# Kernel tuning notes

Hardware: AMD Instinct MI355X
Metric: run time of the kernel (lower is better)

## Reference

```python
import jax, jax.numpy as jnp
import numpy as np

B, T, DE, DR, H = 8192, 8, 512, 1024, 1024


def setup_inputs() -> dict:
    key = jax.random.key(0)
    ks = jax.random.split(key, 8)
    std = 1.0 / np.sqrt(H)
    u = lambda k, shape: jax.random.uniform(k, shape, jnp.float32, -std, std)
    return {
        "entity": jax.random.normal(ks[0], (B, T, DE), jnp.float32),
        "relation": jax.random.normal(ks[1], (B, T, DR), jnp.float32),
        "We": u(ks[2], (H, DE)),
        "be": u(ks[3], (H,)),
        "Wr": u(ks[4], (H, DR)),
        "br": u(ks[5], (H,)),
        "Wh": u(ks[6], (H, H)),
        "bh": u(ks[7], (H,)),
    }


def reference(entity, relation, We, be, Wr, br, Wh, bh):
    # entity: [B, T, DE], relation: [B, T, DR]
    # Precompute time-parallel input projections (linear, math-equivalent to per-step).
    g = (jnp.einsum("btd,hd->bth", entity, We) + be
         + jnp.einsum("btd,hd->bth", relation, Wr) + br)  # [B, T, H]

    def step(h, gt):
        h = jax.nn.relu(gt + h @ Wh.T + bh)  # RNNCell_rel: relu(e2h(e)+r2h(r)+h2h(h))
        return h, h

    h0 = jnp.zeros((entity.shape[0], Wh.shape[0]), entity.dtype)
    hn, outs = jax.lax.scan(step, h0, jnp.transpose(g, (1, 0, 2)))  # outs: [T, B, H]
    output = jnp.transpose(outs, (1, 0, 2))  # [B, T, H] (batch-first)
    need = hn.T  # faithful to hidden[0].transpose(0,1): [H, B]
    return output, need
```

## Files before the change

kernel.cpp:

```cpp
#include <hip/hip_runtime.h>
#include <hip/hip_bf16.h>

#define BB 8192
#define TT 8
#define DEe 512
#define DRr 1024
#define HH 1024
#define KG 1536
#define MG 65536

typedef __attribute__((ext_vector_type(8))) __bf16 bf16x8;
typedef __attribute__((ext_vector_type(4))) __bf16 bf16x4;
typedef __attribute__((ext_vector_type(4))) float f32x4;

__device__ __forceinline__ void gld_lds16(const __bf16* g, __bf16* l) {
    __builtin_amdgcn_global_load_lds(
        (const __attribute__((address_space(1))) void*)g,
        (__attribute__((address_space(3))) void*)l, 16, 0, 0);
}

__global__ void pack_ga(const float* __restrict__ ent, const float* __restrict__ rel,
                        __bf16* __restrict__ ga) {
    const int total = MG * (KG / 4);
    const int stride = gridDim.x * blockDim.x;
    for (int g = blockIdx.x * blockDim.x + threadIdx.x; g < total; g += stride) {
        int m = g / 384;
        int c4 = g - m * 384;
        float4 v;
        if (c4 < 128) v = ((const float4*)ent)[(size_t)m * 128 + c4];
        else          v = ((const float4*)rel)[(size_t)m * 256 + (c4 - 128)];
        bf16x4 o = {(__bf16)v.x, (__bf16)v.y, (__bf16)v.z, (__bf16)v.w};
        *(bf16x4*)(ga + (size_t)m * KG + c4 * 4) = o;
    }
}

__global__ void pack_bw(const float* __restrict__ We, const float* __restrict__ Wr,
                        const float* __restrict__ Wh,
                        __bf16* __restrict__ BW, __bf16* __restrict__ WhP) {
    const int n = blockIdx.y;
    const int sec = blockIdx.x;
    const int i = threadIdx.x;
    float4 v; __bf16* dst;
    if (sec == 0) {
        v = *(const float4*)(We + (size_t)n * DEe + i * 4);
        dst = BW + (size_t)n * KG + i * 4;
    } else if (sec <= 2) {
        int d = (sec - 1) * 512 + i * 4;
        v = *(const float4*)(Wr + (size_t)n * DRr + d);
        dst = BW + (size_t)n * KG + DEe + d;
    } else {
        int d = (sec - 3) * 512 + i * 4;
        v = *(const float4*)(Wh + (size_t)n * HH + d);
        dst = WhP + (size_t)n * HH + d;
    }
    bf16x4 o = {(__bf16)v.x, (__bf16)v.y, (__bf16)v.z, (__bf16)v.w};
    *(bf16x4*)dst = o;
}

__global__ __launch_bounds__(256) void gemm_g(
    const __bf16* __restrict__ A, const __bf16* __restrict__ Bw,
    const float* __restrict__ be, const float* __restrict__ br,
    const float* __restrict__ bh,
    float* __restrict__ out, __bf16* __restrict__ h0) {
    __shared__ __bf16 sA[128 * 32];
    __shared__ __bf16 sB[128 * 32];
    __shared__ float sBias[128];

    const int tid  = threadIdx.x;
    const int lane = tid & 63;
    const int w    = tid >> 6;
    const int bid  = blockIdx.y * 8 + blockIdx.x;
    const int swz  = (bid & 7) * 512 + (bid >> 3);
    const int tileN = (swz & 7) * 128;
    const int tileM = (swz >> 3) * 128;

    if (tid < 128) {
        int n = tileN + tid;
        sBias[tid] = be[n] + br[n] + bh[n];
    }

    const int r0 = (w * 2 + 0) * 16 + (lane >> 2);
    const int r1 = (w * 2 + 1) * 16 + (lane >> 2);
    const int cc = (lane & 3) * 8;
    const __bf16* gA0 = A + (size_t)(tileM + r0) * KG + cc;
    const __bf16* gA1 = A + (size_t)(tileM + r1) * KG + cc;
    const __bf16* gB0 = Bw + (size_t)(tileN + r0) * KG + cc;
    const __bf16* gB1 = Bw + (size_t)(tileN + r1) * KG + cc;
    __bf16* lA0 = sA + (w * 2 + 0) * 512;
    __bf16* lA1 = sA + (w * 2 + 1) * 512;
    __bf16* lB0 = sB + (w * 2 + 0) * 512;
    __bf16* lB1 = sB + (w * 2 + 1) * 512;

    const int wm = (w >> 1) * 64, wn = (w & 1) * 64;
    const int fm = lane & 15, fq = lane >> 4;

    f32x4 acc[4][4];
#pragma unroll
    for (int i = 0; i < 4; i++)
#pragma unroll
        for (int j = 0; j < 4; j++) acc[i][j] = {0.f, 0.f, 0.f, 0.f};

    for (int k0 = 0; k0 < KG; k0 += 32) {
        gld_lds16(gA0 + k0, lA0);
        gld_lds16(gA1 + k0, lA1);
        gld_lds16(gB0 + k0, lB0);
        gld_lds16(gB1 + k0, lB1);
        __syncthreads();
        bf16x8 af[4], bf[4];
#pragma unroll
        for (int mf = 0; mf < 4; mf++)
            af[mf] = *(const bf16x8*)&sA[(wm + mf * 16 + fm) * 32 + fq * 8];
#pragma unroll
        for (int nf = 0; nf < 4; nf++)
            bf[nf] = *(const bf16x8*)&sB[(wn + nf * 16 + fm) * 32 + fq * 8];
#pragma unroll
        for (int mf = 0; mf < 4; mf++)
#pragma unroll
            for (int nf = 0; nf < 4; nf++)
                acc[mf][nf] = __builtin_amdgcn_mfma_f32_16x16x32_bf16(
                    af[mf], bf[nf], acc[mf][nf], 0, 0, 0);
        __syncthreads();
    }

#pragma unroll
    for (int mf = 0; mf < 4; mf++) {
#pragma unroll
        for (int nf = 0; nf < 4; nf++) {
            f32x4 v = acc[mf][nf];
            const int nl = wn + nf * 16 + fm;
            const int n  = tileN + nl;
            const int m0 = tileM + wm + mf * 16 + fq * 4;
            const float bias = sBias[nl];
            const bool t0row = ((m0 & 7) == 0);
#pragma unroll
            for (int r = 0; r < 4; r++) {
                float x = v[r] + bias;
                size_t m = (size_t)(m0 + r);
                if (t0row && r == 0) {
                    float hv = x > 0.f ? x : 0.f;
                    out[m * HH + n] = hv;
                    h0[(m >> 3) * HH + n] = (__bf16)hv;
                } else {
                    out[m * HH + n] = x;
                }
            }
        }
    }
}

__global__ __launch_bounds__(256) void gemm_step(
    const __bf16* __restrict__ A, const __bf16* __restrict__ Bw,
    float* __restrict__ out, __bf16* __restrict__ hn,
    float* __restrict__ need, int t) {
    __shared__ __bf16 sA[128 * 32];
    __shared__ __bf16 sB[128 * 32];

    const int tid  = threadIdx.x;
    const int lane = tid & 63;
    const int w    = tid >> 6;
    const int bid  = blockIdx.y * 8 + blockIdx.x;
    const int swz  = (bid & 7) * 64 + (bid >> 3);
    const int tileN = (swz & 7) * 128;
    const int tileM = (swz >> 3) * 128;

    const int r0 = (w * 2 + 0) * 16 + (lane >> 2);
    const int r1 = (w * 2 + 1) * 16 + (lane >> 2);
    const int cc = (lane & 3) * 8;
    const __bf16* gA0 = A + (size_t)(tileM + r0) * HH + cc;
    const __bf16* gA1 = A + (size_t)(tileM + r1) * HH + cc;
    const __bf16* gB0 = Bw + (size_t)(tileN + r0) * HH + cc;
    const __bf16* gB1 = Bw + (size_t)(tileN + r1) * HH + cc;
    __bf16* lA0 = sA + (w * 2 + 0) * 512;
    __bf16* lA1 = sA + (w * 2 + 1) * 512;
    __bf16* lB0 = sB + (w * 2 + 0) * 512;
    __bf16* lB1 = sB + (w * 2 + 1) * 512;

    const int wm = (w >> 1) * 64, wn = (w & 1) * 64;
    const int fm = lane & 15, fq = lane >> 4;

    f32x4 acc[4][4];
#pragma unroll
    for (int i = 0; i < 4; i++)
#pragma unroll
        for (int j = 0; j < 4; j++) acc[i][j] = {0.f, 0.f, 0.f, 0.f};

    for (int k0 = 0; k0 < HH; k0 += 32) {
        gld_lds16(gA0 + k0, lA0);
        gld_lds16(gA1 + k0, lA1);
        gld_lds16(gB0 + k0, lB0);
        gld_lds16(gB1 + k0, lB1);
        __syncthreads();
        bf16x8 af[4], bf[4];
#pragma unroll
        for (int mf = 0; mf < 4; mf++)
            af[mf] = *(const bf16x8*)&sA[(wm + mf * 16 + fm) * 32 + fq * 8];
#pragma unroll
        for (int nf = 0; nf < 4; nf++)
            bf[nf] = *(const bf16x8*)&sB[(wn + nf * 16 + fm) * 32 + fq * 8];
#pragma unroll
        for (int mf = 0; mf < 4; mf++)
#pragma unroll
            for (int nf = 0; nf < 4; nf++)
                acc[mf][nf] = __builtin_amdgcn_mfma_f32_16x16x32_bf16(
                    af[mf], bf[nf], acc[mf][nf], 0, 0, 0);
        __syncthreads();
    }

#pragma unroll
    for (int mf = 0; mf < 4; mf++) {
#pragma unroll
        for (int nf = 0; nf < 4; nf++) {
            f32x4 v = acc[mf][nf];
            const int nl = wn + nf * 16 + fm;
            const int n  = tileN + nl;
            const int m0 = tileM + wm + mf * 16 + fq * 4;
            float hv[4];
#pragma unroll
            for (int r = 0; r < 4; r++) {
                size_t addr = ((size_t)(m0 + r) * TT + t) * HH + n;
                float x = v[r] + out[addr];
                hv[r] = x > 0.f ? x : 0.f;
                out[addr] = hv[r];
                if (hn) hn[(size_t)(m0 + r) * HH + n] = (__bf16)hv[r];
            }
            if (need) {
                f32x4 nv = {hv[0], hv[1], hv[2], hv[3]};
                *(f32x4*)&need[(size_t)n * BB + m0] = nv;
            }
        }
    }
}

extern "C" void kernel_launch(void* const* d_in, const int* in_sizes, int n_in,
                              void* d_out, int out_size, void* d_ws, size_t ws_size,
                              hipStream_t stream) {
    const float* ent = (const float*)d_in[0];
    const float* rel = (const float*)d_in[1];
    const float* We  = (const float*)d_in[2];
    const float* be  = (const float*)d_in[3];
    const float* Wr  = (const float*)d_in[4];
    const float* br  = (const float*)d_in[5];
    const float* Wh  = (const float*)d_in[6];
    const float* bh  = (const float*)d_in[7];

    float* out  = (float*)d_out;
    float* need = out + (size_t)BB * TT * HH;

    char* ws = (char*)d_ws;
    __bf16* GA  = (__bf16*)ws;
    __bf16* BW  = (__bf16*)(ws + (size_t)MG * KG * 2);
    __bf16* WhP = (__bf16*)(ws + (size_t)MG * KG * 2 + (size_t)HH * KG * 2);
    __bf16* hA  = (__bf16*)((char*)WhP + (size_t)HH * HH * 2);
    __bf16* hB  = (__bf16*)((char*)hA + (size_t)BB * HH * 2);
    __bf16* hbuf[2] = {hA, hB};

    pack_bw<<<dim3(5, 1024), 128, 0, stream>>>(We, Wr, Wh, BW, WhP);
    pack_ga<<<dim3(2048), 256, 0, stream>>>(ent, rel, GA);
    gemm_g<<<dim3(8, 512), 256, 0, stream>>>(GA, BW, be, br, bh, out, hA);
    for (int t = 1; t < TT; t++) {
        gemm_step<<<dim3(8, 64), 256, 0, stream>>>(
            hbuf[(t - 1) & 1], WhP, out,
            (t < 7) ? hbuf[t & 1] : nullptr,
            (t == 7) ? need : nullptr, t);
    }
}
```

Baseline: 1.286 ms.

## Fuse recurrent steps into one persistent kernel keeping hidden state in LDS

Replaces the seven per-timestep GEMM launches with a single kernel in which each block owns 32 batch rows, keeps their hidden state in swizzled LDS as bf16, and loops over all timesteps. Wh is pre-packed into a k-major tiled layout so each k-chunk can be streamed into LDS with plain vector loads. This removes the global round-trips of the hidden state and the per-step launch overhead. In exchange, every block re-streams the full Wh on every step (256 blocks, 512 threads, 128KB LDS, one block per CU), which leans heavily on L2 and gives lower MFMA reuse per Wh byte.

```diff
diff --git a/kernel.cpp b/kernel.cpp
--- a/kernel.cpp
+++ b/kernel.cpp
@@ -36,7 +36,7 @@
 
 __global__ void pack_bw(const float* __restrict__ We, const float* __restrict__ Wr,
                         const float* __restrict__ Wh,
-                        __bf16* __restrict__ BW, __bf16* __restrict__ WhP) {
+                        __bf16* __restrict__ BW, __bf16* __restrict__ WhT) {
     const int n = blockIdx.y;
     const int sec = blockIdx.x;
     const int i = threadIdx.x;
@@ -51,7 +51,7 @@
     } else {
         int d = (sec - 3) * 512 + i * 4;
         v = *(const float4*)(Wh + (size_t)n * HH + d);
-        dst = WhP + (size_t)n * HH + d;
+        dst = WhT + (d >> 5) * 32768 + ((d >> 3) & 3) * 8192 + n * 8 + (d & 7);
     }
     bf16x4 o = {(__bf16)v.x, (__bf16)v.y, (__bf16)v.z, (__bf16)v.w};
     *(bf16x4*)dst = o;
@@ -60,8 +60,7 @@
 __global__ __launch_bounds__(256) void gemm_g(
     const __bf16* __restrict__ A, const __bf16* __restrict__ Bw,
     const float* __restrict__ be, const float* __restrict__ br,
-    const float* __restrict__ bh,
-    float* __restrict__ out, __bf16* __restrict__ h0) {
+    const float* __restrict__ bh, float* __restrict__ out) {
     __shared__ __bf16 sA[128 * 32];
     __shared__ __bf16 sB[128 * 32];
     __shared__ float sBias[128];
@@ -106,19 +105,19 @@
         gld_lds16(gB0 + k0, lB0);
         gld_lds16(gB1 + k0, lB1);
         __syncthreads();
-        bf16x8 af[4], bf[4];
+        bf16x8 af[4], bfv[4];
 #pragma unroll
         for (int mf = 0; mf < 4; mf++)
             af[mf] = *(const bf16x8*)&sA[(wm + mf * 16 + fm) * 32 + fq * 8];
 #pragma unroll
         for (int nf = 0; nf < 4; nf++)
-            bf[nf] = *(const bf16x8*)&sB[(wn + nf * 16 + fm) * 32 + fq * 8];
+            bfv[nf] = *(const bf16x8*)&sB[(wn + nf * 16 + fm) * 32 + fq * 8];
 #pragma unroll
         for (int mf = 0; mf < 4; mf++)
 #pragma unroll
             for (int nf = 0; nf < 4; nf++)
                 acc[mf][nf] = __builtin_amdgcn_mfma_f32_16x16x32_bf16(
-                    af[mf], bf[nf], acc[mf][nf], 0, 0, 0);
+                    af[mf], bfv[nf], acc[mf][nf], 0, 0, 0);
         __syncthreads();
     }
 
@@ -137,9 +136,7 @@
                 float x = v[r] + bias;
                 size_t m = (size_t)(m0 + r);
                 if (t0row && r == 0) {
-                    float hv = x > 0.f ? x : 0.f;
-                    out[m * HH + n] = hv;
-                    h0[(m >> 3) * HH + n] = (__bf16)hv;
+                    out[m * HH + n] = x > 0.f ? x : 0.f;
                 } else {
                     out[m * HH + n] = x;
                 }
@@ -148,86 +145,99 @@
     }
 }
 
-__global__ __launch_bounds__(256) void gemm_step(
-    const __bf16* __restrict__ A, const __bf16* __restrict__ Bw,
-    float* __restrict__ out, __bf16* __restrict__ hn,
-    float* __restrict__ need, int t) {
-    __shared__ __bf16 sA[128 * 32];
-    __shared__ __bf16 sB[128 * 32];
+__global__ __launch_bounds__(512, 1) void rnn_local(
+    const __bf16* __restrict__ Bw,
+    float* __restrict__ out, float* __restrict__ need) {
+    __shared__ __bf16 sH[32 * 1024];
+    __shared__ __bf16 sB[32 * 1024];
 
     const int tid  = threadIdx.x;
     const int lane = tid & 63;
     const int w    = tid >> 6;
-    const int bid  = blockIdx.y * 8 + blockIdx.x;
-    const int swz  = (bid & 7) * 64 + (bid >> 3);
-    const int tileN = (swz & 7) * 128;
-    const int tileM = (swz >> 3) * 128;
-
-    const int r0 = (w * 2 + 0) * 16 + (lane >> 2);
-    const int r1 = (w * 2 + 1) * 16 + (lane >> 2);
-    const int cc = (lane & 3) * 8;
-    const __bf16* gA0 = A + (size_t)(tileM + r0) * HH + cc;
-    const __bf16* gA1 = A + (size_t)(tileM + r1) * HH + cc;
-    const __bf16* gB0 = Bw + (size_t)(tileN + r0) * HH + cc;
-    const __bf16* gB1 = Bw + (size_t)(tileN + r1) * HH + cc;
-    __bf16* lA0 = sA + (w * 2 + 0) * 512;
-    __bf16* lA1 = sA + (w * 2 + 1) * 512;
-    __bf16* lB0 = sB + (w * 2 + 0) * 512;
-    __bf16* lB1 = sB + (w * 2 + 1) * 512;
-
-    const int wm = (w >> 1) * 64, wn = (w & 1) * 64;
-    const int fm = lane & 15, fq = lane >> 4;
-
-    f32x4 acc[4][4];
-#pragma unroll
-    for (int i = 0; i < 4; i++)
-#pragma unroll
-        for (int j = 0; j < 4; j++) acc[i][j] = {0.f, 0.f, 0.f, 0.f};
-
-    for (int k0 = 0; k0 < HH; k0 += 32) {
-        gld_lds16(gA0 + k0, lA0);
-        gld_lds16(gA1 + k0, lA1);
-        gld_lds16(gB0 + k0, lB0);
-        gld_lds16(gB1 + k0, lB1);
+    const int b0   = blockIdx.x * 32;
+    const int fm   = lane & 15, fq = lane >> 4;
+    const int wn   = w * 128;
+
+#pragma unroll
+    for (int i = 0; i < 8; i++) {
+        int c  = i * 512 + tid;
+        int m  = c >> 7;
+        int cc = (c & 127) * 8;
+        const float* src = out + ((size_t)(b0 + m) * TT + 0) * HH + cc;
+        float4 v0 = *(const float4*)src;
+        float4 v1 = *(const float4*)(src + 4);
+        bf16x8 o = {(__bf16)v0.x, (__bf16)v0.y, (__bf16)v0.z, (__bf16)v0.w,
+                    (__bf16)v1.x, (__bf16)v1.y, (__bf16)v1.z, (__bf16)v1.w};
+        int byte = (m * 2048 + cc * 2) ^ ((m & 7) << 4);
+        *(bf16x8*)((char*)sH + byte) = o;
+    }
+    __syncthreads();
+
+    for (int t = 1; t < TT; t++) {
+        f32x4 acc[2][8];
+#pragma unroll
+        for (int i = 0; i < 2; i++)
+#pragma unroll
+            for (int j = 0; j < 8; j++) acc[i][j] = {0.f, 0.f, 0.f, 0.f};
+
+        for (int k0i = 0; k0i < 32; k0i++) {
+            const __bf16* gsrc = Bw + (size_t)k0i * 32768;
+            float4 stg[8];
+#pragma unroll
+            for (int j = 0; j < 8; j++)
+                stg[j] = *(const float4*)(gsrc + ((size_t)(j * 512 + tid)) * 8);
+#pragma unroll
+            for (int j = 0; j < 8; j++)
+                *(float4*)(sB + (size_t)(j * 512 + tid) * 8) = stg[j];
+            __syncthreads();
+
+            bf16x8 af[2], bfv[8];
+            const int kb = k0i * 64;
+#pragma unroll
+            for (int mf = 0; mf < 2; mf++) {
+                int m = mf * 16 + fm;
+                int byte = (m * 2048 + kb + fq * 16) ^ ((m & 7) << 4);
+                af[mf] = *(const bf16x8*)((const char*)sH + byte);
+            }
+#pragma unroll
+            for (int nf = 0; nf < 8; nf++) {
+                int n = wn + nf * 16 + fm;
+                bfv[nf] = *(const bf16x8*)((const char*)sB + (fq * 1024 + n) * 16);
+            }
+#pragma unroll
+            for (int mf = 0; mf < 2; mf++)
+#pragma unroll
+                for (int nf = 0; nf < 8; nf++)
+                    acc[mf][nf] = __builtin_amdgcn_mfma_f32_16x16x32_bf16(
+                        af[mf], bfv[nf], acc[mf][nf], 0, 0, 0);
+            __syncthreads();
+        }
+
+#pragma unroll
+        for (int mf = 0; mf < 2; mf++) {
+#pragma unroll
+            for (int nf = 0; nf < 8; nf++) {
+                f32x4 v = acc[mf][nf];
+                const int n  = wn + nf * 16 + fm;
+                const int m0 = mf * 16 + fq * 4;
+                float hv[4];
+#pragma unroll
+                for (int r = 0; r < 4; r++) {
+                    int m = m0 + r;
+                    size_t addr = ((size_t)(b0 + m) * TT + t) * HH + n;
+                    float x = v[r] + out[addr];
+                    hv[r] = x > 0.f ? x : 0.f;
+                    out[addr] = hv[r];
+                    int byte = (m * 2048 + n * 2) ^ ((m & 7) << 4);
+                    *(__bf16*)((char*)sH + byte) = (__bf16)hv[r];
+                }
+                if (t == 7) {
+                    f32x4 nv = {hv[0], hv[1], hv[2], hv[3]};
+                    *(f32x4*)&need[(size_t)n * BB + b0 + m0] = nv;
+                }
+            }
+        }
         __syncthreads();
-        bf16x8 af[4], bf[4];
-#pragma unroll
-        for (int mf = 0; mf < 4; mf++)
-            af[mf] = *(const bf16x8*)&sA[(wm + mf * 16 + fm) * 32 + fq * 8];
-#pragma unroll
-        for (int nf = 0; nf < 4; nf++)
-            bf[nf] = *(const bf16x8*)&sB[(wn + nf * 16 + fm) * 32 + fq * 8];
-#pragma unroll
-        for (int mf = 0; mf < 4; mf++)
-#pragma unroll
-            for (int nf = 0; nf < 4; nf++)
-                acc[mf][nf] = __builtin_amdgcn_mfma_f32_16x16x32_bf16(
-                    af[mf], bf[nf], acc[mf][nf], 0, 0, 0);
-        __syncthreads();
-    }
-
-#pragma unroll
-    for (int mf = 0; mf < 4; mf++) {
-#pragma unroll
-        for (int nf = 0; nf < 4; nf++) {
-            f32x4 v = acc[mf][nf];
-            const int nl = wn + nf * 16 + fm;
-            const int n  = tileN + nl;
-            const int m0 = tileM + wm + mf * 16 + fq * 4;
-            float hv[4];
-#pragma unroll
-            for (int r = 0; r < 4; r++) {
-                size_t addr = ((size_t)(m0 + r) * TT + t) * HH + n;
-                float x = v[r] + out[addr];
-                hv[r] = x > 0.f ? x : 0.f;
-                out[addr] = hv[r];
-                if (hn) hn[(size_t)(m0 + r) * HH + n] = (__bf16)hv[r];
-            }
-            if (need) {
-                f32x4 nv = {hv[0], hv[1], hv[2], hv[3]};
-                *(f32x4*)&need[(size_t)n * BB + m0] = nv;
-            }
-        }
     }
 }
 
@@ -249,18 +259,10 @@
     char* ws = (char*)d_ws;
     __bf16* GA  = (__bf16*)ws;
     __bf16* BW  = (__bf16*)(ws + (size_t)MG * KG * 2);
-    __bf16* WhP = (__bf16*)(ws + (size_t)MG * KG * 2 + (size_t)HH * KG * 2);
-    __bf16* hA  = (__bf16*)((char*)WhP + (size_t)HH * HH * 2);
-    __bf16* hB  = (__bf16*)((char*)hA + (size_t)BB * HH * 2);
-    __bf16* hbuf[2] = {hA, hB};
-
-    pack_bw<<<dim3(5, 1024), 128, 0, stream>>>(We, Wr, Wh, BW, WhP);
+    __bf16* WhT = (__bf16*)(ws + (size_t)MG * KG * 2 + (size_t)HH * KG * 2);
+
+    pack_bw<<<dim3(5, 1024), 128, 0, stream>>>(We, Wr, Wh, BW, WhT);
     pack_ga<<<dim3(2048), 256, 0, stream>>>(ent, rel, GA);
-    gemm_g<<<dim3(8, 512), 256, 0, stream>>>(GA, BW, be, br, bh, out, hA);
-    for (int t = 1; t < TT; t++) {
-        gemm_step<<<dim3(8, 64), 256, 0, stream>>>(
-            hbuf[(t - 1) & 1], WhP, out,
-            (t < 7) ? hbuf[t & 1] : nullptr,
-            (t == 7) ? need : nullptr, t);
-    }
-}
+    gemm_g<<<dim3(8, 512), 256, 0, stream>>>(GA, BW, be, br, bh, out);
+    rnn_local<<<dim3(256), dim3(512), 0, stream>>>(WhT, out, need);
+}
```

After: 1.209 ms. 6.0% less time.
